# Kernel optimization log

Measured on AMD Instinct MI355X. Metric: run time of the kernel, lower is better.

## Reference

```python
import jax, jax.numpy as jnp
import numpy as np

D_MODEL = 512
NUM_HEADS = 8
DEPTH = D_MODEL // NUM_HEADS
MAX_SEQ = 2048
B, L = 4, 1024


def setup_inputs() -> dict:
    key = jax.random.key(0)
    ks = jax.random.split(key, 13)
    s = 0.02
    return {
        "v": jax.random.normal(ks[0], (B, L, D_MODEL), jnp.float32),
        "k": jax.random.normal(ks[1], (B, L, D_MODEL), jnp.float32),
        "q": jax.random.normal(ks[2], (B, L, D_MODEL), jnp.float32),
        "mask": jnp.zeros((1, 1, L, L), jnp.float32),
        "wq_w": jax.random.normal(ks[3], (D_MODEL, D_MODEL), jnp.float32) * s,
        "wq_b": jnp.zeros((D_MODEL,), jnp.float32),
        "wk_w": jax.random.normal(ks[4], (D_MODEL, D_MODEL), jnp.float32) * s,
        "wk_b": jnp.zeros((D_MODEL,), jnp.float32),
        "wv_w": jax.random.normal(ks[5], (D_MODEL, D_MODEL), jnp.float32) * s,
        "wv_b": jnp.zeros((D_MODEL,), jnp.float32),
        "wo_w": jax.random.normal(ks[6], (D_MODEL, D_MODEL), jnp.float32) * s,
        "wo_b": jnp.zeros((D_MODEL,), jnp.float32),
        "pos_emb": jax.random.normal(ks[7], (MAX_SEQ, DEPTH), jnp.float32) * s,
    }


def _split_heads(x, batch):
    # [B, L, d_model] -> [B, H, L, depth]
    return x.reshape(batch, -1, NUM_HEADS, DEPTH).transpose(0, 2, 1, 3)


def reference(v, k, q, mask, wq_w, wq_b, wk_w, wk_b, wv_w, wv_b, wo_w, wo_b, pos_emb):
    batch, l_q, _ = q.shape
    qh = _split_heads(q @ wq_w + wq_b, batch)   # [B,H,Lq,depth]
    kh = _split_heads(k @ wk_w + wk_b, batch)   # [B,H,Lk,depth]
    vh = _split_heads(v @ wv_w + wv_b, batch)   # [B,H,Lk,depth]
    l_k = kh.shape[2]

    # relative position embedding slice: last l_q rows of pos_emb -> [Lq, depth]
    e = pos_emb[max(0, MAX_SEQ - l_q):, :]
    qe = jnp.einsum('nhld,md->nhlm', qh, e)     # [B,H,Lq,Lq]

    # upper-left triangular masking: keep entries with i + j >= Lq - 1
    keep = (jnp.arange(l_q)[:, None] + jnp.arange(l_q)[None, :]) >= (l_q - 1)
    qe = qe * keep.astype(qe.dtype)

    # skew trick: pad left on last dim, reshape [L, L+1]->[L+1, L], drop first row
    padded = jnp.pad(qe, ((0, 0), (0, 0), (0, 0), (1, 0)))
    srel = padded.reshape(batch, NUM_HEADS, l_q + 1, l_q)[:, :, 1:, :]  # [B,H,Lq,Lq]
    if l_k > l_q:
        srel = jnp.pad(srel, ((0, 0), (0, 0), (0, 0), (0, l_k - l_q)))
    elif l_k < l_q:
        srel = srel[..., :l_k]

    scale = 1.0 / jnp.sqrt(jnp.asarray(DEPTH, qh.dtype))
    logits = (jnp.einsum('nhld,nhmd->nhlm', qh, kh) + srel) * scale
    logits = logits + mask * (-1e9)
    attn = jax.nn.softmax(logits, axis=-1)      # [B,H,Lq,Lk]
    ctx = jnp.einsum('nhlm,nhmd->nhld', attn, vh)
    ctx = ctx.transpose(0, 2, 1, 3).reshape(batch, l_q, D_MODEL)
    out = ctx @ wo_w + wo_b
    return out, attn
```

## Files before the change

### kernel.cpp

```cpp
#include <hip/hip_runtime.h>

typedef __attribute__((ext_vector_type(4))) float f32x4;
typedef __attribute__((ext_vector_type(8))) short s16x8;
typedef __attribute__((ext_vector_type(4))) unsigned short u16x4;

__device__ inline unsigned short f2bf(float f) {
  unsigned int u = __builtin_bit_cast(unsigned int, f);
  u += 0x7fff + ((u >> 16) & 1);
  return (unsigned short)(u >> 16);
}
__device__ inline float bf2f(unsigned short u) {
  return __builtin_bit_cast(float, (unsigned int)u << 16);
}

__device__ __forceinline__ void async16(const void* g, void* s) {
  __builtin_amdgcn_global_load_lds(
      (const __attribute__((address_space(1))) unsigned int*)g,
      (__attribute__((address_space(3))) unsigned int*)s, 16, 0, 0);
}

__global__ __launch_bounds__(256) void cast_kernel(
    const float* __restrict__ v, const float* __restrict__ k, const float* __restrict__ q,
    const float* __restrict__ wq, const float* __restrict__ wk, const float* __restrict__ wv,
    const float* __restrict__ wo, const float* __restrict__ pos,
    unsigned short* __restrict__ qbf, unsigned short* __restrict__ kbf,
    unsigned short* __restrict__ vbf, unsigned short* __restrict__ wqT,
    unsigned short* __restrict__ wkT, unsigned short* __restrict__ wvT,
    unsigned short* __restrict__ woT, unsigned short* __restrict__ ebf) {
  int seg = blockIdx.y;
  int tid = blockIdx.x * blockDim.x + threadIdx.x;
  int stride = gridDim.x * blockDim.x;
  if (seg < 3) {
    const float* src = seg == 0 ? q : (seg == 1 ? k : v);
    unsigned short* dst = seg == 0 ? qbf : (seg == 1 ? kbf : vbf);
    for (int i = tid; i < 4096 * 512 / 4; i += stride) {
      f32x4 x = *(const f32x4*)&src[i * 4];
      u16x4 o = {f2bf(x[0]), f2bf(x[1]), f2bf(x[2]), f2bf(x[3])};
      *(u16x4*)&dst[i * 4] = o;
    }
  } else if (seg < 7) {
    const float* src = seg == 3 ? wq : seg == 4 ? wk : seg == 5 ? wv : wo;
    unsigned short* dst = seg == 3 ? wqT : seg == 4 ? wkT : seg == 5 ? wvT : woT;
    for (int i = tid; i < 512 * 128; i += stride) {
      int n = i >> 7, k0 = (i & 127) * 4;
      u16x4 o = {f2bf(src[(k0 + 0) * 512 + n]), f2bf(src[(k0 + 1) * 512 + n]),
                 f2bf(src[(k0 + 2) * 512 + n]), f2bf(src[(k0 + 3) * 512 + n])};
      *(u16x4*)&dst[n * 512 + k0] = o;
    }
  } else {
    for (int i = tid; i < 1024 * 64 / 4; i += stride) {
      f32x4 x = *(const f32x4*)&pos[1024 * 64 + i * 4];
      u16x4 o = {f2bf(x[0]), f2bf(x[1]), f2bf(x[2]), f2bf(x[3])};
      *(u16x4*)&ebf[i * 4] = o;
    }
  }
}

__device__ __forceinline__ void gemm_main(
    const unsigned short* __restrict__ A, const unsigned short* __restrict__ Bt,
    unsigned short* As, unsigned short* Bs, int r0, int c0, int tid,
    f32x4 acc[4][4]) {
  int lane = tid & 63, w = tid >> 6;
  int wr = w >> 1, wc = w & 1;
  int frow = lane & 15, kg = lane >> 4;
  for (int k0 = 0; k0 < 512; k0 += 32) {
#pragma unroll
    for (int j = 0; j < 2; ++j) {
      int t = tid + j * 256;
      int row = t >> 2, col = (t & 3) * 8;
      *(s16x8*)&As[row * 32 + col] = *(const s16x8*)&A[(size_t)(r0 + row) * 512 + k0 + col];
      *(s16x8*)&Bs[row * 32 + col] = *(const s16x8*)&Bt[(size_t)(c0 + row) * 512 + k0 + col];
    }
    __syncthreads();
    s16x8 af[4], bfr[4];
#pragma unroll
    for (int mi = 0; mi < 4; ++mi) af[mi] = *(s16x8*)&As[(wr * 64 + mi * 16 + frow) * 32 + kg * 8];
#pragma unroll
    for (int ni = 0; ni < 4; ++ni) bfr[ni] = *(s16x8*)&Bs[(wc * 64 + ni * 16 + frow) * 32 + kg * 8];
#pragma unroll
    for (int mi = 0; mi < 4; ++mi)
#pragma unroll
      for (int ni = 0; ni < 4; ++ni)
        acc[mi][ni] = __builtin_amdgcn_mfma_f32_16x16x32_bf16(af[mi], bfr[ni], acc[mi][ni], 0, 0, 0);
    __syncthreads();
  }
}

__global__ __launch_bounds__(256, 2) void proj3_kernel(
    const unsigned short* __restrict__ qbf, const unsigned short* __restrict__ kbf,
    const unsigned short* __restrict__ vbf, const unsigned short* __restrict__ wqT,
    const unsigned short* __restrict__ wkT, const unsigned short* __restrict__ wvT,
    const float* __restrict__ wq_b, const float* __restrict__ wk_b,
    const float* __restrict__ wv_b, unsigned short* __restrict__ qhw,
    unsigned short* __restrict__ khw, unsigned short* __restrict__ vhT) {
  __shared__ unsigned short As[128 * 32];
  __shared__ unsigned short Bs[128 * 32];
  int z = blockIdx.z;
  const unsigned short* A = z == 0 ? qbf : z == 1 ? kbf : vbf;
  const unsigned short* Bt = z == 0 ? wqT : z == 1 ? wkT : wvT;
  const float* bias = z == 0 ? wq_b : z == 1 ? wk_b : wv_b;
  unsigned short* outp = z == 0 ? qhw : z == 1 ? khw : vhT;
  int r0 = blockIdx.x * 128, c0 = blockIdx.y * 128;
  int tid = threadIdx.x;
  int lane = tid & 63, w = tid >> 6;
  int wr = w >> 1, wc = w & 1;
  int frow = lane & 15, kg = lane >> 4;
  f32x4 acc[4][4] = {};
  gemm_main(A, Bt, As, Bs, r0, c0, tid, acc);
#pragma unroll
  for (int ni = 0; ni < 4; ++ni) {
    int gc = c0 + wc * 64 + ni * 16 + frow;
    float bi = bias[gc];
#pragma unroll
    for (int mi = 0; mi < 4; ++mi) {
#pragma unroll
      for (int reg = 0; reg < 4; ++reg) {
        int gr = r0 + wr * 64 + mi * 16 + kg * 4 + reg;
        float val = acc[mi][ni][reg] + bi;
        if (z != 2) {
          outp[(size_t)((gr >> 10) * 8 + (gc >> 6)) * 65536 +
               (size_t)(gr & 1023) * 64 + (gc & 63)] = f2bf(val);
        } else {
          outp[(size_t)((gr >> 10) * 8 + (gc >> 6)) * 65536 +
               (size_t)(gc & 63) * 1024 + (gr & 1023)] = f2bf(val);
        }
      }
    }
  }
}

__global__ __launch_bounds__(256, 2) void gemm_out_kernel(
    const unsigned short* __restrict__ A, const unsigned short* __restrict__ Bt,
    const float* __restrict__ bias, float* __restrict__ outp) {
  __shared__ unsigned short As[128 * 32];
  __shared__ unsigned short Bs[128 * 32];
  int r0 = blockIdx.x * 128, c0 = blockIdx.y * 128;
  int tid = threadIdx.x;
  int lane = tid & 63, w = tid >> 6;
  int wr = w >> 1, wc = w & 1;
  int frow = lane & 15, kg = lane >> 4;
  f32x4 acc[4][4] = {};
  gemm_main(A, Bt, As, Bs, r0, c0, tid, acc);
#pragma unroll
  for (int ni = 0; ni < 4; ++ni) {
    int gc = c0 + wc * 64 + ni * 16 + frow;
    float bi = bias[gc];
#pragma unroll
    for (int mi = 0; mi < 4; ++mi)
#pragma unroll
      for (int reg = 0; reg < 4; ++reg) {
        int gr = r0 + wr * 64 + mi * 16 + kg * 4 + reg;
        outp[(size_t)gr * 512 + gc] = acc[mi][ni][reg] + bi;
      }
  }
}

__global__ __launch_bounds__(512, 2) void attn_kernel(
    const unsigned short* __restrict__ qh, const unsigned short* __restrict__ kh,
    const unsigned short* __restrict__ vhT, const unsigned short* __restrict__ ebf,
    const float* __restrict__ mask, float* __restrict__ attn_out,
    unsigned short* __restrict__ ctx) {
  __shared__ unsigned short S[16 * 1024];
  __shared__ unsigned short KV[2][8192];
  __shared__ float redmax[8][16], redsum[8][16];
  __shared__ float ctxred[4][16][16];
  int fid = blockIdx.x;
  int nh = ((fid & 7) << 2) | ((fid >> 3) & 3);
  int l0 = (fid >> 5) << 4;
  int tid = threadIdx.x;
  int lane = tid & 63, w = tid >> 6;
  int frow = lane & 15, kg = lane >> 4;

  auto sp = [&](int r, int c) -> unsigned short* {
    int byte = (r << 11) + (c << 1);
    byte ^= (r & 7) << 4;
    return (unsigned short*)((char*)S + byte);
  };

  auto stageKE = [&](const unsigned short* srcbase, int buf) {
#pragma unroll
    for (int i = 0; i < 2; ++i) {
      int u = i * 64 + lane;
      int row = u >> 3, p = u & 7;
      async16(srcbase + (size_t)(w * 16 + row) * 64 + ((p ^ (row & 7)) * 8),
              &KV[buf][w * 1024 + i * 512]);
    }
  };
  auto stageV = [&](const unsigned short* vsrc, int c, int buf) {
    int mh = w >> 2, dg = w & 3;
#pragma unroll
    for (int i = 0; i < 2; ++i) {
      int u = i * 64 + lane;
      int row = u >> 3, p = u & 7;
      async16(vsrc + (size_t)(dg * 16 + row) * 1024 + mh * 512 + c * 64 + ((p ^ (row & 7)) * 8),
              &KV[buf][w * 1024 + i * 512]);
    }
  };

  const unsigned short* qbase = qh + ((size_t)nh * 1024 + l0 + frow) * 64 + kg * 8;
  s16x8 qf0 = *(const s16x8*)(qbase);
  s16x8 qf1 = *(const s16x8*)(qbase + 32);

  int cmin = 1008 - l0;
  int cstart = cmin >> 7;
  stageKE(ebf + (size_t)cstart * 8192, cstart & 1);
  if (cstart + 1 < 8) stageKE(ebf + (size_t)(cstart + 1) * 8192, (cstart + 1) & 1);
  for (int c = cstart; c < 8; ++c) {
    int buf = c & 1;
    if (c + 1 < 8) { asm volatile("s_waitcnt vmcnt(2)" ::: "memory"); }
    else           { asm volatile("s_waitcnt vmcnt(0)" ::: "memory"); }
    __builtin_amdgcn_sched_barrier(0);
    int j0 = c * 128 + w * 16;
    if (j0 + 15 >= cmin) {
      const char* base = (const char*)&KV[buf][0] + w * 2048 + frow * 128;
      s16x8 b0 = *(const s16x8*)(base + ((kg ^ (frow & 7)) << 4));
      s16x8 b1 = *(const s16x8*)(base + (((4 + kg) ^ (frow & 7)) << 4));
      f32x4 a = {};
      a = __builtin_amdgcn_mfma_f32_16x16x32_bf16(b0, qf0, a, 0, 0, 0);
      a = __builtin_amdgcn_mfma_f32_16x16x32_bf16(b1, qf1, a, 0, 0, 0);
      u16x4 pk = {f2bf(a[0]), f2bf(a[1]), f2bf(a[2]), f2bf(a[3])};
      *(u16x4*)sp(frow, j0 + kg * 4) = pk;
    }
    asm volatile("s_waitcnt lgkmcnt(0)" ::: "memory");
    __builtin_amdgcn_sched_barrier(0);
    if (c + 2 < 8) stageKE(ebf + (size_t)(c + 2) * 8192, buf);
  }
  const unsigned short* kbase = kh + (size_t)nh * 65536;
  stageKE(kbase, 0);
  stageKE(kbase + 8192, 1);
  __syncthreads();

  f32x4 lg[8];
#pragma unroll
  for (int c = 0; c < 8; ++c) {
    int buf = c & 1;
    if (c + 1 < 8) { asm volatile("s_waitcnt vmcnt(2)" ::: "memory"); }
    else           { asm volatile("s_waitcnt vmcnt(0)" ::: "memory"); }
    __builtin_amdgcn_sched_barrier(0);
    const char* base = (const char*)&KV[buf][0] + w * 2048 + frow * 128;
    s16x8 b0 = *(const s16x8*)(base + ((kg ^ (frow & 7)) << 4));
    s16x8 b1 = *(const s16x8*)(base + (((4 + kg) ^ (frow & 7)) << 4));
    f32x4 a = {};
    a = __builtin_amdgcn_mfma_f32_16x16x32_bf16(b0, qf0, a, 0, 0, 0);
    a = __builtin_amdgcn_mfma_f32_16x16x32_bf16(b1, qf1, a, 0, 0, 0);
    lg[c] = a;
    asm volatile("s_waitcnt lgkmcnt(0)" ::: "memory");
    __builtin_amdgcn_sched_barrier(0);
    if (c + 2 < 8) stageKE(kbase + (size_t)(c + 2) * 8192, buf);
  }

  const unsigned short* vsrc = vhT + (size_t)nh * 65536;
  stageV(vsrc, 0, 0);
  stageV(vsrc, 1, 1);

  int lq = l0 + frow;
#pragma unroll
  for (int c = 0; c < 8; ++c) {
    int m0k = c * 128 + w * 16 + kg * 4;
    f32x4 mk = *(const f32x4*)&mask[(size_t)lq * 1024 + m0k];
#pragma unroll
    for (int reg = 0; reg < 4; ++reg) {
      int m = m0k + reg;
      float srel = (m <= lq) ? bf2f(*sp(frow, 1023 + m - lq)) : 0.f;
      lg[c][reg] = (lg[c][reg] + srel) * 0.125f + mk[reg] * -1e9f;
    }
  }

  f32x4 vmax = lg[0];
#pragma unroll
  for (int c = 1; c < 8; ++c) {
#pragma unroll
    for (int reg = 0; reg < 4; ++reg) vmax[reg] = fmaxf(vmax[reg], lg[c][reg]);
  }
  float mx = fmaxf(fmaxf(vmax[0], vmax[1]), fmaxf(vmax[2], vmax[3]));
  mx = fmaxf(mx, __shfl_xor(mx, 16));
  mx = fmaxf(mx, __shfl_xor(mx, 32));
  float s = 0.f;
#pragma unroll
  for (int c = 0; c < 8; ++c) {
#pragma unroll
    for (int reg = 0; reg < 4; ++reg) {
      lg[c][reg] = __expf(lg[c][reg] - mx);
      s += lg[c][reg];
    }
  }
  s += __shfl_xor(s, 16);
  s += __shfl_xor(s, 32);
  if (lane < 16) {
    redmax[w][lane] = mx;
    redsum[w][lane] = s;
  }
  __syncthreads();

  float gmax = redmax[0][frow];
#pragma unroll
  for (int wv = 1; wv < 8; ++wv) gmax = fmaxf(gmax, redmax[wv][frow]);
  float gsum = 0.f;
#pragma unroll
  for (int wv = 0; wv < 8; ++wv) gsum += redsum[wv][frow] * __expf(redmax[wv][frow] - gmax);
  float fac = __expf(mx - gmax) / gsum;

  size_t arow = ((size_t)nh * 1024 + lq) * 1024;
#pragma unroll
  for (int c = 0; c < 8; ++c) {
    int m0k = c * 128 + w * 16 + kg * 4;
    f32x4 pn;
#pragma unroll
    for (int reg = 0; reg < 4; ++reg) pn[reg] = lg[c][reg] * fac;
    *(f32x4*)&attn_out[arow + m0k] = pn;
    u16x4 pb = {f2bf(pn[0]), f2bf(pn[1]), f2bf(pn[2]), f2bf(pn[3])};
    *(u16x4*)sp(frow, m0k) = pb;
  }
  __syncthreads();

  {
    int mh = w >> 2, dg = w & 3;
    f32x4 acc = {};
#pragma unroll
    for (int c = 0; c < 8; ++c) {
      int buf = c & 1;
      if (c + 1 < 8) { asm volatile("s_waitcnt vmcnt(2)" ::: "memory"); }
      else           { asm volatile("s_waitcnt vmcnt(0)" ::: "memory"); }
      __builtin_amdgcn_sched_barrier(0);
      const char* vbase = (const char*)&KV[buf][0] + w * 2048 + frow * 128;
#pragma unroll
      for (int ks = 0; ks < 2; ++ks) {
        s16x8 a = *(s16x8*)sp(frow, mh * 512 + c * 64 + ks * 32 + kg * 8);
        s16x8 b = *(const s16x8*)(vbase + (((ks * 4 + kg) ^ (frow & 7)) << 4));
        acc = __builtin_amdgcn_mfma_f32_16x16x32_bf16(a, b, acc, 0, 0, 0);
      }
      asm volatile("s_waitcnt lgkmcnt(0)" ::: "memory");
      __builtin_amdgcn_sched_barrier(0);
      if (c + 2 < 8) stageV(vsrc, c + 2, buf);
    }
    if (w >= 4) {
#pragma unroll
      for (int reg = 0; reg < 4; ++reg) ctxred[dg][kg * 4 + reg][frow] = acc[reg];
    }
    __syncthreads();
    if (w < 4) {
      int n = nh >> 3, h = nh & 7;
#pragma unroll
      for (int reg = 0; reg < 4; ++reg) {
        float val = acc[reg] + ctxred[dg][kg * 4 + reg][frow];
        ctx[((size_t)(n * 1024 + l0 + kg * 4 + reg)) * 512 + h * 64 + dg * 16 + frow] =
            f2bf(val);
      }
    }
  }
}

extern "C" void kernel_launch(void* const* d_in, const int* in_sizes, int n_in,
                              void* d_out, int out_size, void* d_ws, size_t ws_size,
                              hipStream_t stream) {
  const float* v = (const float*)d_in[0];
  const float* k = (const float*)d_in[1];
  const float* q = (const float*)d_in[2];
  const float* mask = (const float*)d_in[3];
  const float* wq_w = (const float*)d_in[4];
  const float* wq_b = (const float*)d_in[5];
  const float* wk_w = (const float*)d_in[6];
  const float* wk_b = (const float*)d_in[7];
  const float* wv_w = (const float*)d_in[8];
  const float* wv_b = (const float*)d_in[9];
  const float* wo_w = (const float*)d_in[10];
  const float* wo_b = (const float*)d_in[11];
  const float* pos = (const float*)d_in[12];

  float* outp = (float*)d_out;
  float* attn_out = outp + (size_t)4 * 1024 * 512;

  char* ws = (char*)d_ws;
  unsigned short* qbf = (unsigned short*)(ws);
  unsigned short* kbf = (unsigned short*)(ws + ((size_t)4 << 20));
  unsigned short* vbf = (unsigned short*)(ws + ((size_t)8 << 20));
  unsigned short* wqT = (unsigned short*)(ws + ((size_t)12 << 20));
  unsigned short* wkT = (unsigned short*)(ws + ((size_t)12 << 20) + (512 << 10));
  unsigned short* wvT = (unsigned short*)(ws + ((size_t)13 << 20));
  unsigned short* woT = (unsigned short*)(ws + ((size_t)13 << 20) + (512 << 10));
  unsigned short* ebf = (unsigned short*)(ws + ((size_t)14 << 20));
  unsigned short* qhw = (unsigned short*)(ws + ((size_t)16 << 20));
  unsigned short* khw = (unsigned short*)(ws + ((size_t)20 << 20));
  unsigned short* vhT = (unsigned short*)(ws + ((size_t)24 << 20));
  unsigned short* ctx = qbf;

  cast_kernel<<<dim3(256, 8), 256, 0, stream>>>(v, k, q, wq_w, wk_w, wv_w, wo_w, pos,
                                                qbf, kbf, vbf, wqT, wkT, wvT, woT, ebf);
  proj3_kernel<<<dim3(32, 4, 3), 256, 0, stream>>>(qbf, kbf, vbf, wqT, wkT, wvT,
                                                   wq_b, wk_b, wv_b, qhw, khw, vhT);
  attn_kernel<<<2048, 512, 0, stream>>>(qhw, khw, vhT, ebf, mask, attn_out, ctx);
  gemm_out_kernel<<<dim3(32, 4), 256, 0, stream>>>(ctx, woT, wo_b, outp);
}
```

Baseline: 123.3 us.

## Halve attention block to four waves and drop cross-wave ctx reduction

Result: slower. 140.6 us (+14.1%).

```diff
diff --git a/kernel.cpp b/kernel.cpp
--- a/kernel.cpp
+++ b/kernel.cpp
@@ -155,15 +155,14 @@
   }
 }
 
-__global__ __launch_bounds__(512, 2) void attn_kernel(
+__global__ __launch_bounds__(256, 2) void attn_kernel(
     const unsigned short* __restrict__ qh, const unsigned short* __restrict__ kh,
     const unsigned short* __restrict__ vhT, const unsigned short* __restrict__ ebf,
     const float* __restrict__ mask, float* __restrict__ attn_out,
     unsigned short* __restrict__ ctx) {
   __shared__ unsigned short S[16 * 1024];
-  __shared__ unsigned short KV[2][8192];
-  __shared__ float redmax[8][16], redsum[8][16];
-  __shared__ float ctxred[4][16][16];
+  __shared__ unsigned short KV[2][4096];
+  __shared__ float redmax[4][16], redsum[4][16];
   int fid = blockIdx.x;
   int nh = ((fid & 7) << 2) | ((fid >> 3) & 3);
   int l0 = (fid >> 5) << 4;
@@ -180,19 +179,18 @@
   auto stageKE = [&](const unsigned short* srcbase, int buf) {
 #pragma unroll
     for (int i = 0; i < 2; ++i) {
-      int u = i * 64 + lane;
-      int row = u >> 3, p = u & 7;
-      async16(srcbase + (size_t)(w * 16 + row) * 64 + ((p ^ (row & 7)) * 8),
+      int rl = i * 8 + (lane >> 3);
+      int p = lane & 7;
+      async16(srcbase + (size_t)(w * 16 + rl) * 64 + ((p ^ (rl & 7)) * 8),
               &KV[buf][w * 1024 + i * 512]);
     }
   };
   auto stageV = [&](const unsigned short* vsrc, int c, int buf) {
-    int mh = w >> 2, dg = w & 3;
 #pragma unroll
     for (int i = 0; i < 2; ++i) {
-      int u = i * 64 + lane;
-      int row = u >> 3, p = u & 7;
-      async16(vsrc + (size_t)(dg * 16 + row) * 1024 + mh * 512 + c * 64 + ((p ^ (row & 7)) * 8),
+      int rl = i * 8 + (lane >> 3);
+      int p = lane & 7;
+      async16(vsrc + (size_t)(w * 16 + rl) * 1024 + c * 64 + ((p ^ (rl & 7)) * 8),
               &KV[buf][w * 1024 + i * 512]);
     }
   };
@@ -202,15 +200,15 @@
   s16x8 qf1 = *(const s16x8*)(qbase + 32);
 
   int cmin = 1008 - l0;
-  int cstart = cmin >> 7;
-  stageKE(ebf + (size_t)cstart * 8192, cstart & 1);
-  if (cstart + 1 < 8) stageKE(ebf + (size_t)(cstart + 1) * 8192, (cstart + 1) & 1);
-  for (int c = cstart; c < 8; ++c) {
+  int cstart = cmin >> 6;
+  stageKE(ebf + (size_t)cstart * 4096, cstart & 1);
+  if (cstart + 1 < 16) stageKE(ebf + (size_t)(cstart + 1) * 4096, (cstart + 1) & 1);
+  for (int c = cstart; c < 16; ++c) {
     int buf = c & 1;
-    if (c + 1 < 8) { asm volatile("s_waitcnt vmcnt(2)" ::: "memory"); }
-    else           { asm volatile("s_waitcnt vmcnt(0)" ::: "memory"); }
+    if (c + 1 < 16) { asm volatile("s_waitcnt vmcnt(2)" ::: "memory"); }
+    else            { asm volatile("s_waitcnt vmcnt(0)" ::: "memory"); }
     __builtin_amdgcn_sched_barrier(0);
-    int j0 = c * 128 + w * 16;
+    int j0 = c * 64 + w * 16;
     if (j0 + 15 >= cmin) {
       const char* base = (const char*)&KV[buf][0] + w * 2048 + frow * 128;
       s16x8 b0 = *(const s16x8*)(base + ((kg ^ (frow & 7)) << 4));
@@ -223,19 +221,19 @@
     }
     asm volatile("s_waitcnt lgkmcnt(0)" ::: "memory");
     __builtin_amdgcn_sched_barrier(0);
-    if (c + 2 < 8) stageKE(ebf + (size_t)(c + 2) * 8192, buf);
+    if (c + 2 < 16) stageKE(ebf + (size_t)(c + 2) * 4096, buf);
   }
   const unsigned short* kbase = kh + (size_t)nh * 65536;
   stageKE(kbase, 0);
-  stageKE(kbase + 8192, 1);
+  stageKE(kbase + 4096, 1);
   __syncthreads();
 
-  f32x4 lg[8];
-#pragma unroll
-  for (int c = 0; c < 8; ++c) {
+  f32x4 lg[16];
+#pragma unroll
+  for (int c = 0; c < 16; ++c) {
     int buf = c & 1;
-    if (c + 1 < 8) { asm volatile("s_waitcnt vmcnt(2)" ::: "memory"); }
-    else           { asm volatile("s_waitcnt vmcnt(0)" ::: "memory"); }
+    if (c + 1 < 16) { asm volatile("s_waitcnt vmcnt(2)" ::: "memory"); }
+    else            { asm volatile("s_waitcnt vmcnt(0)" ::: "memory"); }
     __builtin_amdgcn_sched_barrier(0);
     const char* base = (const char*)&KV[buf][0] + w * 2048 + frow * 128;
     s16x8 b0 = *(const s16x8*)(base + ((kg ^ (frow & 7)) << 4));
@@ -246,17 +244,13 @@
     lg[c] = a;
     asm volatile("s_waitcnt lgkmcnt(0)" ::: "memory");
     __builtin_amdgcn_sched_barrier(0);
-    if (c + 2 < 8) stageKE(kbase + (size_t)(c + 2) * 8192, buf);
-  }
-
-  const unsigned short* vsrc = vhT + (size_t)nh * 65536;
-  stageV(vsrc, 0, 0);
-  stageV(vsrc, 1, 1);
+    if (c + 2 < 16) stageKE(kbase + (size_t)(c + 2) * 4096, buf);
+  }
 
   int lq = l0 + frow;
 #pragma unroll
-  for (int c = 0; c < 8; ++c) {
-    int m0k = c * 128 + w * 16 + kg * 4;
+  for (int c = 0; c < 16; ++c) {
+    int m0k = c * 64 + w * 16 + kg * 4;
     f32x4 mk = *(const f32x4*)&mask[(size_t)lq * 1024 + m0k];
 #pragma unroll
     for (int reg = 0; reg < 4; ++reg) {
@@ -268,7 +262,7 @@
 
   f32x4 vmax = lg[0];
 #pragma unroll
-  for (int c = 1; c < 8; ++c) {
+  for (int c = 1; c < 16; ++c) {
 #pragma unroll
     for (int reg = 0; reg < 4; ++reg) vmax[reg] = fmaxf(vmax[reg], lg[c][reg]);
   }
@@ -277,7 +271,7 @@
   mx = fmaxf(mx, __shfl_xor(mx, 32));
   float s = 0.f;
 #pragma unroll
-  for (int c = 0; c < 8; ++c) {
+  for (int c = 0; c < 16; ++c) {
 #pragma unroll
     for (int reg = 0; reg < 4; ++reg) {
       lg[c][reg] = __expf(lg[c][reg] - mx);
@@ -292,18 +286,18 @@
   }
   __syncthreads();
 
-  float gmax = redmax[0][frow];
-#pragma unroll
-  for (int wv = 1; wv < 8; ++wv) gmax = fmaxf(gmax, redmax[wv][frow]);
-  float gsum = 0.f;
-#pragma unroll
-  for (int wv = 0; wv < 8; ++wv) gsum += redsum[wv][frow] * __expf(redmax[wv][frow] - gmax);
+  float gmax = fmaxf(fmaxf(redmax[0][frow], redmax[1][frow]),
+                     fmaxf(redmax[2][frow], redmax[3][frow]));
+  float gsum = redsum[0][frow] * __expf(redmax[0][frow] - gmax) +
+               redsum[1][frow] * __expf(redmax[1][frow] - gmax) +
+               redsum[2][frow] * __expf(redmax[2][frow] - gmax) +
+               redsum[3][frow] * __expf(redmax[3][frow] - gmax);
   float fac = __expf(mx - gmax) / gsum;
 
   size_t arow = ((size_t)nh * 1024 + lq) * 1024;
 #pragma unroll
-  for (int c = 0; c < 8; ++c) {
-    int m0k = c * 128 + w * 16 + kg * 4;
+  for (int c = 0; c < 16; ++c) {
+    int m0k = c * 64 + w * 16 + kg * 4;
     f32x4 pn;
 #pragma unroll
     for (int reg = 0; reg < 4; ++reg) pn[reg] = lg[c][reg] * fac;
@@ -311,41 +305,35 @@
     u16x4 pb = {f2bf(pn[0]), f2bf(pn[1]), f2bf(pn[2]), f2bf(pn[3])};
     *(u16x4*)sp(frow, m0k) = pb;
   }
+  const unsigned short* vsrc = vhT + (size_t)nh * 65536;
+  stageV(vsrc, 0, 0);
+  stageV(vsrc, 1, 1);
   __syncthreads();
 
   {
-    int mh = w >> 2, dg = w & 3;
     f32x4 acc = {};
 #pragma unroll
-    for (int c = 0; c < 8; ++c) {
+    for (int c = 0; c < 16; ++c) {
       int buf = c & 1;
-      if (c + 1 < 8) { asm volatile("s_waitcnt vmcnt(2)" ::: "memory"); }
-      else           { asm volatile("s_waitcnt vmcnt(0)" ::: "memory"); }
+      if (c + 1 < 16) { asm volatile("s_waitcnt vmcnt(2)" ::: "memory"); }
+      else            { asm volatile("s_waitcnt vmcnt(0)" ::: "memory"); }
       __builtin_amdgcn_sched_barrier(0);
       const char* vbase = (const char*)&KV[buf][0] + w * 2048 + frow * 128;
 #pragma unroll
       for (int ks = 0; ks < 2; ++ks) {
-        s16x8 a = *(s16x8*)sp(frow, mh * 512 + c * 64 + ks * 32 + kg * 8);
+        s16x8 a = *(s16x8*)sp(frow, c * 64 + ks * 32 + kg * 8);
         s16x8 b = *(const s16x8*)(vbase + (((ks * 4 + kg) ^ (frow & 7)) << 4));
         acc = __builtin_amdgcn_mfma_f32_16x16x32_bf16(a, b, acc, 0, 0, 0);
       }
       asm volatile("s_waitcnt lgkmcnt(0)" ::: "memory");
       __builtin_amdgcn_sched_barrier(0);
-      if (c + 2 < 8) stageV(vsrc, c + 2, buf);
-    }
-    if (w >= 4) {
-#pragma unroll
-      for (int reg = 0; reg < 4; ++reg) ctxred[dg][kg * 4 + reg][frow] = acc[reg];
-    }
-    __syncthreads();
-    if (w < 4) {
-      int n = nh >> 3, h = nh & 7;
-#pragma unroll
-      for (int reg = 0; reg < 4; ++reg) {
-        float val = acc[reg] + ctxred[dg][kg * 4 + reg][frow];
-        ctx[((size_t)(n * 1024 + l0 + kg * 4 + reg)) * 512 + h * 64 + dg * 16 + frow] =
-            f2bf(val);
-      }
+      if (c + 2 < 16) stageV(vsrc, c + 2, buf);
+    }
+    int n = nh >> 3, h = nh & 7;
+#pragma unroll
+    for (int reg = 0; reg < 4; ++reg) {
+      int rr = kg * 4 + reg;
+      ctx[((size_t)(n * 1024 + l0 + rr)) * 512 + h * 64 + w * 16 + frow] = f2bf(acc[reg]);
     }
   }
 }
@@ -388,6 +376,6 @@
                                                 qbf, kbf, vbf, wqT, wkT, wvT, woT, ebf);
   proj3_kernel<<<dim3(32, 4, 3), 256, 0, stream>>>(qbf, kbf, vbf, wqT, wkT, wvT,
                                                    wq_b, wk_b, wv_b, qhw, khw, vhT);
-  attn_kernel<<<2048, 512, 0, stream>>>(qhw, khw, vhT, ebf, mask, attn_out, ctx);
+  attn_kernel<<<2048, 256, 0, stream>>>(qhw, khw, vhT, ebf, mask, attn_out, ctx);
   gemm_out_kernel<<<dim3(32, 4), 256, 0, stream>>>(ctx, woT, wo_b, outp);
 }
```

## Fuse fp32-to-bf16 activation cast into projection GEMM loads

Applied to the files above, without the earlier changes.

Result: faster. 118.8 us (median of 2 runs) (-3.6%).

```diff
diff --git a/kernel.cpp b/kernel.cpp
--- a/kernel.cpp
+++ b/kernel.cpp
@@ -20,27 +20,17 @@
 }
 
 __global__ __launch_bounds__(256) void cast_kernel(
-    const float* __restrict__ v, const float* __restrict__ k, const float* __restrict__ q,
     const float* __restrict__ wq, const float* __restrict__ wk, const float* __restrict__ wv,
     const float* __restrict__ wo, const float* __restrict__ pos,
-    unsigned short* __restrict__ qbf, unsigned short* __restrict__ kbf,
-    unsigned short* __restrict__ vbf, unsigned short* __restrict__ wqT,
-    unsigned short* __restrict__ wkT, unsigned short* __restrict__ wvT,
-    unsigned short* __restrict__ woT, unsigned short* __restrict__ ebf) {
+    unsigned short* __restrict__ wqT, unsigned short* __restrict__ wkT,
+    unsigned short* __restrict__ wvT, unsigned short* __restrict__ woT,
+    unsigned short* __restrict__ ebf) {
   int seg = blockIdx.y;
   int tid = blockIdx.x * blockDim.x + threadIdx.x;
   int stride = gridDim.x * blockDim.x;
-  if (seg < 3) {
-    const float* src = seg == 0 ? q : (seg == 1 ? k : v);
-    unsigned short* dst = seg == 0 ? qbf : (seg == 1 ? kbf : vbf);
-    for (int i = tid; i < 4096 * 512 / 4; i += stride) {
-      f32x4 x = *(const f32x4*)&src[i * 4];
-      u16x4 o = {f2bf(x[0]), f2bf(x[1]), f2bf(x[2]), f2bf(x[3])};
-      *(u16x4*)&dst[i * 4] = o;
-    }
-  } else if (seg < 7) {
-    const float* src = seg == 3 ? wq : seg == 4 ? wk : seg == 5 ? wv : wo;
-    unsigned short* dst = seg == 3 ? wqT : seg == 4 ? wkT : seg == 5 ? wvT : woT;
+  if (seg < 4) {
+    const float* src = seg == 0 ? wq : seg == 1 ? wk : seg == 2 ? wv : wo;
+    unsigned short* dst = seg == 0 ? wqT : seg == 1 ? wkT : seg == 2 ? wvT : woT;
     for (int i = tid; i < 512 * 128; i += stride) {
       int n = i >> 7, k0 = (i & 127) * 4;
       u16x4 o = {f2bf(src[(k0 + 0) * 512 + n]), f2bf(src[(k0 + 1) * 512 + n]),
@@ -56,39 +46,9 @@
   }
 }
 
-__device__ __forceinline__ void gemm_main(
-    const unsigned short* __restrict__ A, const unsigned short* __restrict__ Bt,
-    unsigned short* As, unsigned short* Bs, int r0, int c0, int tid,
-    f32x4 acc[4][4]) {
-  int lane = tid & 63, w = tid >> 6;
-  int wr = w >> 1, wc = w & 1;
-  int frow = lane & 15, kg = lane >> 4;
-  for (int k0 = 0; k0 < 512; k0 += 32) {
-#pragma unroll
-    for (int j = 0; j < 2; ++j) {
-      int t = tid + j * 256;
-      int row = t >> 2, col = (t & 3) * 8;
-      *(s16x8*)&As[row * 32 + col] = *(const s16x8*)&A[(size_t)(r0 + row) * 512 + k0 + col];
-      *(s16x8*)&Bs[row * 32 + col] = *(const s16x8*)&Bt[(size_t)(c0 + row) * 512 + k0 + col];
-    }
-    __syncthreads();
-    s16x8 af[4], bfr[4];
-#pragma unroll
-    for (int mi = 0; mi < 4; ++mi) af[mi] = *(s16x8*)&As[(wr * 64 + mi * 16 + frow) * 32 + kg * 8];
-#pragma unroll
-    for (int ni = 0; ni < 4; ++ni) bfr[ni] = *(s16x8*)&Bs[(wc * 64 + ni * 16 + frow) * 32 + kg * 8];
-#pragma unroll
-    for (int mi = 0; mi < 4; ++mi)
-#pragma unroll
-      for (int ni = 0; ni < 4; ++ni)
-        acc[mi][ni] = __builtin_amdgcn_mfma_f32_16x16x32_bf16(af[mi], bfr[ni], acc[mi][ni], 0, 0, 0);
-    __syncthreads();
-  }
-}
-
 __global__ __launch_bounds__(256, 2) void proj3_kernel(
-    const unsigned short* __restrict__ qbf, const unsigned short* __restrict__ kbf,
-    const unsigned short* __restrict__ vbf, const unsigned short* __restrict__ wqT,
+    const float* __restrict__ qf, const float* __restrict__ kf,
+    const float* __restrict__ vf, const unsigned short* __restrict__ wqT,
     const unsigned short* __restrict__ wkT, const unsigned short* __restrict__ wvT,
     const float* __restrict__ wq_b, const float* __restrict__ wk_b,
     const float* __restrict__ wv_b, unsigned short* __restrict__ qhw,
@@ -96,7 +56,7 @@
   __shared__ unsigned short As[128 * 32];
   __shared__ unsigned short Bs[128 * 32];
   int z = blockIdx.z;
-  const unsigned short* A = z == 0 ? qbf : z == 1 ? kbf : vbf;
+  const float* A = z == 0 ? qf : z == 1 ? kf : vf;
   const unsigned short* Bt = z == 0 ? wqT : z == 1 ? wkT : wvT;
   const float* bias = z == 0 ? wq_b : z == 1 ? wk_b : wv_b;
   unsigned short* outp = z == 0 ? qhw : z == 1 ? khw : vhT;
@@ -106,7 +66,32 @@
   int wr = w >> 1, wc = w & 1;
   int frow = lane & 15, kg = lane >> 4;
   f32x4 acc[4][4] = {};
-  gemm_main(A, Bt, As, Bs, r0, c0, tid, acc);
+  for (int k0 = 0; k0 < 512; k0 += 32) {
+#pragma unroll
+    for (int j = 0; j < 2; ++j) {
+      int t = tid + j * 256;
+      int row = t >> 2, col = (t & 3) * 8;
+      f32x4 a0 = *(const f32x4*)&A[(size_t)(r0 + row) * 512 + k0 + col];
+      f32x4 a1 = *(const f32x4*)&A[(size_t)(r0 + row) * 512 + k0 + col + 4];
+      u16x4 p0 = {f2bf(a0[0]), f2bf(a0[1]), f2bf(a0[2]), f2bf(a0[3])};
+      u16x4 p1 = {f2bf(a1[0]), f2bf(a1[1]), f2bf(a1[2]), f2bf(a1[3])};
+      *(u16x4*)&As[row * 32 + col] = p0;
+      *(u16x4*)&As[row * 32 + col + 4] = p1;
+      *(s16x8*)&Bs[row * 32 + col] = *(const s16x8*)&Bt[(size_t)(c0 + row) * 512 + k0 + col];
+    }
+    __syncthreads();
+    s16x8 af[4], bfr[4];
+#pragma unroll
+    for (int mi = 0; mi < 4; ++mi) af[mi] = *(s16x8*)&As[(wr * 64 + mi * 16 + frow) * 32 + kg * 8];
+#pragma unroll
+    for (int ni = 0; ni < 4; ++ni) bfr[ni] = *(s16x8*)&Bs[(wc * 64 + ni * 16 + frow) * 32 + kg * 8];
+#pragma unroll
+    for (int mi = 0; mi < 4; ++mi)
+#pragma unroll
+      for (int ni = 0; ni < 4; ++ni)
+        acc[mi][ni] = __builtin_amdgcn_mfma_f32_16x16x32_bf16(af[mi], bfr[ni], acc[mi][ni], 0, 0, 0);
+    __syncthreads();
+  }
 #pragma unroll
   for (int ni = 0; ni < 4; ++ni) {
     int gc = c0 + wc * 64 + ni * 16 + frow;
@@ -140,7 +125,27 @@
   int wr = w >> 1, wc = w & 1;
   int frow = lane & 15, kg = lane >> 4;
   f32x4 acc[4][4] = {};
-  gemm_main(A, Bt, As, Bs, r0, c0, tid, acc);
+  for (int k0 = 0; k0 < 512; k0 += 32) {
+#pragma unroll
+    for (int j = 0; j < 2; ++j) {
+      int t = tid + j * 256;
+      int row = t >> 2, col = (t & 3) * 8;
+      *(s16x8*)&As[row * 32 + col] = *(const s16x8*)&A[(size_t)(r0 + row) * 512 + k0 + col];
+      *(s16x8*)&Bs[row * 32 + col] = *(const s16x8*)&Bt[(size_t)(c0 + row) * 512 + k0 + col];
+    }
+    __syncthreads();
+    s16x8 af[4], bfr[4];
+#pragma unroll
+    for (int mi = 0; mi < 4; ++mi) af[mi] = *(s16x8*)&As[(wr * 64 + mi * 16 + frow) * 32 + kg * 8];
+#pragma unroll
+    for (int ni = 0; ni < 4; ++ni) bfr[ni] = *(s16x8*)&Bs[(wc * 64 + ni * 16 + frow) * 32 + kg * 8];
+#pragma unroll
+    for (int mi = 0; mi < 4; ++mi)
+#pragma unroll
+      for (int ni = 0; ni < 4; ++ni)
+        acc[mi][ni] = __builtin_amdgcn_mfma_f32_16x16x32_bf16(af[mi], bfr[ni], acc[mi][ni], 0, 0, 0);
+    __syncthreads();
+  }
 #pragma unroll
   for (int ni = 0; ni < 4; ++ni) {
     int gc = c0 + wc * 64 + ni * 16 + frow;
@@ -249,10 +254,6 @@
     if (c + 2 < 8) stageKE(kbase + (size_t)(c + 2) * 8192, buf);
   }
 
-  const unsigned short* vsrc = vhT + (size_t)nh * 65536;
-  stageV(vsrc, 0, 0);
-  stageV(vsrc, 1, 1);
-
   int lq = l0 + frow;
 #pragma unroll
   for (int c = 0; c < 8; ++c) {
@@ -314,6 +315,9 @@
   __syncthreads();
 
   {
+    const unsigned short* vsrc = vhT + (size_t)nh * 65536;
+    stageV(vsrc, 0, 0);
+    stageV(vsrc, 1, 1);
     int mh = w >> 2, dg = w & 3;
     f32x4 acc = {};
 #pragma unroll
@@ -371,9 +375,7 @@
   float* attn_out = outp + (size_t)4 * 1024 * 512;
 
   char* ws = (char*)d_ws;
-  unsigned short* qbf = (unsigned short*)(ws);
-  unsigned short* kbf = (unsigned short*)(ws + ((size_t)4 << 20));
-  unsigned short* vbf = (unsigned short*)(ws + ((size_t)8 << 20));
+  unsigned short* ctx = (unsigned short*)(ws);
   unsigned short* wqT = (unsigned short*)(ws + ((size_t)12 << 20));
   unsigned short* wkT = (unsigned short*)(ws + ((size_t)12 << 20) + (512 << 10));
   unsigned short* wvT = (unsigned short*)(ws + ((size_t)13 << 20));
@@ -382,11 +384,10 @@
   unsigned short* qhw = (unsigned short*)(ws + ((size_t)16 << 20));
   unsigned short* khw = (unsigned short*)(ws + ((size_t)20 << 20));
   unsigned short* vhT = (unsigned short*)(ws + ((size_t)24 << 20));
-  unsigned short* ctx = qbf;
-
-  cast_kernel<<<dim3(256, 8), 256, 0, stream>>>(v, k, q, wq_w, wk_w, wv_w, wo_w, pos,
-                                                qbf, kbf, vbf, wqT, wkT, wvT, woT, ebf);
-  proj3_kernel<<<dim3(32, 4, 3), 256, 0, stream>>>(qbf, kbf, vbf, wqT, wkT, wvT,
+
+  cast_kernel<<<dim3(256, 5), 256, 0, stream>>>(wq_w, wk_w, wv_w, wo_w, pos,
+                                                wqT, wkT, wvT, woT, ebf);
+  proj3_kernel<<<dim3(32, 4, 3), 256, 0, stream>>>(q, k, v, wqT, wkT, wvT,
                                                    wq_b, wk_b, wv_b, qhw, khw, vhT);
   attn_kernel<<<2048, 512, 0, stream>>>(qhw, khw, vhT, ebf, mask, attn_out, ctx);
   gemm_out_kernel<<<dim3(32, 4), 256, 0, stream>>>(ctx, woT, wo_b, outp);
```
